# Optimization experiments

Measured on AMD Instinct MI355X. Metric: run time of the kernel, lower is better.

The kernel has to match this reference:

```python
import jax, jax.numpy as jnp
import numpy as np

B, T, C, H = 128, 256, 64, 128  # batch, seq_len, num_channels, hidden_size


def setup_inputs() -> dict:
    key = jax.random.key(0)
    ks = jax.random.split(key, 7)
    s = 1.0 / np.sqrt(H)  # PyTorch LSTM/Linear init bound
    x = jax.random.normal(ks[0], (B, T, C), dtype=jnp.float32)
    # Per-channel LSTM weights (input_size=1). Gate order i,f,g,o like PyTorch.
    w_ih = jax.random.uniform(ks[1], (C, 4 * H), jnp.float32, -s, s)      # [C,4H] (input is scalar)
    w_hh = jax.random.uniform(ks[2], (C, 4 * H, H), jnp.float32, -s, s)   # [C,4H,H]
    b_ih = jax.random.uniform(ks[3], (C, 4 * H), jnp.float32, -s, s)
    b_hh = jax.random.uniform(ks[4], (C, 4 * H), jnp.float32, -s, s)
    # Per-channel Linear(H, 1) head.
    w_fc = jax.random.uniform(ks[5], (C, H), jnp.float32, -s, s)
    b_fc = jax.random.uniform(ks[6], (C,), jnp.float32, -s, s)
    return {"x": x, "w_ih": w_ih, "w_hh": w_hh, "b_ih": b_ih,
            "b_hh": b_hh, "w_fc": w_fc, "b_fc": b_fc}


def reference(x, w_ih, w_hh, b_ih, b_hh, w_fc, b_fc):
    # x: [B,T,C]. All C channel-LSTMs run as one batched recurrence over [B,C].
    b = b_ih + b_hh  # [C,4H]
    xt = jnp.transpose(x, (1, 0, 2))  # [T,B,C] for scan over time
    h0 = jnp.zeros((x.shape[0], x.shape[2], w_hh.shape[-1]), x.dtype)  # [B,C,H]
    c0 = h0

    def step(carry, x_t):
        h, c = carry  # [B,C,H]
        # scalar input times per-channel input weights + recurrent GEMM
        gates = x_t[..., None] * w_ih + jnp.einsum('bch,cgh->bcg', h, w_hh) + b  # [B,C,4H]
        i, f, g, o = jnp.split(gates, 4, axis=-1)
        i = jax.nn.sigmoid(i)
        f = jax.nn.sigmoid(f)
        g = jnp.tanh(g)
        o = jax.nn.sigmoid(o)
        c_new = f * c + i * g
        h_new = o * jnp.tanh(c_new)
        return (h_new, c_new), None

    (hT, _), _ = jax.lax.scan(step, (h0, c0), xt)
    # Per-channel linear head on the last hidden state -> [B,C]
    return jnp.einsum('bch,ch->bc', hT, w_fc) + b_fc
```

## Files before the change

### kernel.cpp

```cpp
#include <hip/hip_runtime.h>
#include <hip/hip_bf16.h>

typedef __bf16 bf16_t;
typedef bf16_t bf16x8 __attribute__((ext_vector_type(8)));
typedef float f32x4 __attribute__((ext_vector_type(4)));

#define B_   128
#define T_   256
#define C_   64
#define H_   128
#define G_   512
#define BT   16
#define XS   20
#define HBUF 2048

#define K1 1.4426950408889634f
#define K2 2.8853900817779268f

__global__ __launch_bounds__(512, 4) void lstm_fused(
    const float* __restrict__ x,
    const float* __restrict__ w_ih,
    const float* __restrict__ w_hh,
    const float* __restrict__ b_ih,
    const float* __restrict__ b_hh,
    const float* __restrict__ w_fc,
    const float* __restrict__ b_fc,
    float* __restrict__ out)
{
    const int c    = blockIdx.x & (C_ - 1);
    const int bt   = blockIdx.x >> 6;
    const int b0   = bt * BT;
    const int tid  = threadIdx.x;
    const int w    = tid >> 6;
    const int lane = tid & 63;
    const int l16  = lane & 15;
    const int lg   = lane >> 4;

    __shared__ __align__(16) bf16_t h_lds[2 * HBUF];
    __shared__ __align__(16) float x_lds[T_ * XS];

    for (int i = tid; i < HBUF; i += 512) ((uint32_t*)h_lds)[i] = 0u;
    for (int i = tid; i < BT * T_; i += 512) {
        const int bl = i >> 8, t = i & 255;
        x_lds[t * XS + bl] = x[(size_t)(b0 + bl) * (T_ * C_) + (size_t)t * C_ + c];
    }

    bf16x8 bw[4][4];
    float  bias[4], wih[4];
    #pragma unroll
    for (int q = 0; q < 4; ++q) {
        const int n = q * 128 + w * 16 + l16;
        bias[q] = b_ih[c * G_ + n] + b_hh[c * G_ + n];
        wih[q]  = w_ih[c * G_ + n];
        #pragma unroll
        for (int kk = 0; kk < 4; ++kk) {
            const int k0 = kk * 32 + lg * 8;
            const float4 wa = *(const float4*)&w_hh[((size_t)(c * G_ + n)) * H_ + k0];
            const float4 wb = *(const float4*)&w_hh[((size_t)(c * G_ + n)) * H_ + k0 + 4];
            bf16x8 g;
            g[0] = (bf16_t)wa.x; g[1] = (bf16_t)wa.y; g[2] = (bf16_t)wa.z; g[3] = (bf16_t)wa.w;
            g[4] = (bf16_t)wb.x; g[5] = (bf16_t)wb.y; g[6] = (bf16_t)wb.z; g[7] = (bf16_t)wb.w;
            bw[q][kk] = g;
        }
    }

    float cst[4] = {0.f, 0.f, 0.f, 0.f};

    __syncthreads();

    const int a_off  = l16 * 8;
    const int wbase  = (w * 2 + (l16 >> 3)) * 128 + lg * 32 + (l16 & 7);

    auto step = [&](const int RD, const int WR, const int t) {
        const f32x4 xv = *(const f32x4*)&x_lds[t * XS + lg * 4];

        bf16x8 a[4];
        #pragma unroll
        for (int kk = 0; kk < 4; ++kk)
            a[kk] = *(const bf16x8*)&h_lds[RD + (kk * 4 + lg) * 128 + a_off];

        f32x4 acc[4];
        #pragma unroll
        for (int q = 0; q < 4; ++q)
            #pragma unroll
            for (int r = 0; r < 4; ++r)
                acc[q][r] = fmaf(xv[r], wih[q], bias[q]);

        #pragma unroll
        for (int q = 0; q < 4; ++q)
            #pragma unroll
            for (int kk = 0; kk < 4; ++kk)
                acc[q] = __builtin_amdgcn_mfma_f32_16x16x32_bf16(a[kk], bw[q][kk], acc[q], 0, 0, 0);

        #pragma unroll
        for (int r = 0; r < 4; ++r) {
            const float ei = __builtin_amdgcn_exp2f(-K1 * acc[0][r]);
            const float ef = __builtin_amdgcn_exp2f(-K1 * acc[1][r]);
            const float eg = __builtin_amdgcn_exp2f( K2 * acc[2][r]);
            const float eo = __builtin_amdgcn_exp2f(-K1 * acc[3][r]);
            const float A  = 1.f + ei, D = 1.f + ef, Bb = 1.f + eg, O = 1.f + eo;
            const float AB = A * Bb;
            const float r1 = __builtin_amdgcn_rcpf(D * AB);
            const float cn = fmaf(D, eg - 1.f, cst[r] * AB) * r1;
            cst[r] = cn;
            float m2 = K2 * cn;
            m2 = fminf(fmaxf(m2, -60.f), 60.f);
            const float ec = __builtin_amdgcn_exp2f(m2);
            const float r2 = __builtin_amdgcn_rcpf(O * (1.f + ec));
            const float hv = (ec - 1.f) * r2;
            h_lds[WR + wbase + r * 8] = (bf16_t)hv;
        }
        __syncthreads();
    };

    for (int t = 0; t < T_; t += 2) {
        step(0, HBUF, t);
        step(HBUF, 0, t + 1);
    }

    #pragma unroll
    for (int rr = 0; rr < 2; ++rr) {
        const int row = w * 2 + rr;
        const int eaddr = (lane >> 2) * 128 + row * 8 + (lane & 3) * 2;
        const float h0 = (float)h_lds[eaddr];
        const float h1 = (float)h_lds[eaddr + 1];
        const float2 wf = *(const float2*)&w_fc[c * H_ + 2 * lane];
        float p = h0 * wf.x + h1 * wf.y;
        #pragma unroll
        for (int off = 32; off; off >>= 1) p += __shfl_xor(p, off);
        if (lane == 0) out[(size_t)(b0 + row) * C_ + c] = p + b_fc[c];
    }
}

extern "C" void kernel_launch(void* const* d_in, const int* in_sizes, int n_in,
                              void* d_out, int out_size, void* d_ws, size_t ws_size,
                              hipStream_t stream) {
    const float* x    = (const float*)d_in[0];
    const float* w_ih = (const float*)d_in[1];
    const float* w_hh = (const float*)d_in[2];
    const float* b_ih = (const float*)d_in[3];
    const float* b_hh = (const float*)d_in[4];
    const float* w_fc = (const float*)d_in[5];
    const float* b_fc = (const float*)d_in[6];
    float* out = (float*)d_out;

    dim3 grid(C_ * (B_ / BT));
    dim3 block(512);
    lstm_fused<<<grid, block, 0, stream>>>(x, w_ih, w_hh, b_ih, b_hh, w_fc, b_fc, out);
}
```

Baseline: 387.6 us.

## Fold input projection and bias into an extra MFMA, prescale gate weights

Moves the scalar input times w_ih plus bias term into an additional bf16 MFMA. A and B operands are built from hi/lo bf16 splits of x, w_ih and bias so precision is kept. The activation scales (-log2e, 2log2e) are folded into the weights so the gate nonlinearities skip a multiply. The elementwise math is also rewritten with packed float2 vectors so the compiler can emit packed FP32 ops. This cuts VALU work per step on the serial recurrence path, at the cost of four extra MFMAs and some operand-packing overhead per step.

Measured after the change: 347.5 us. 10.4% less time.

```diff
diff --git a/kernel.cpp b/kernel.cpp
--- a/kernel.cpp
+++ b/kernel.cpp
@@ -4,6 +4,7 @@
 typedef __bf16 bf16_t;
 typedef bf16_t bf16x8 __attribute__((ext_vector_type(8)));
 typedef float f32x4 __attribute__((ext_vector_type(4)));
+typedef float f32x2 __attribute__((ext_vector_type(2)));
 
 #define B_   128
 #define T_   256
@@ -11,11 +12,22 @@
 #define H_   128
 #define G_   512
 #define BT   16
-#define XS   20
 #define HBUF 2048
 
 #define K1 1.4426950408889634f
 #define K2 2.8853900817779268f
+
+union AF { bf16x8 v; uint32_t w[4]; };
+
+__device__ __forceinline__ uint32_t cvt_pk_bf16(float a, float b) {
+    uint32_t r; asm("v_cvt_pk_bf16_f32 %0, %1, %2" : "=v"(r) : "v"(a), "v"(b)); return r;
+}
+__device__ __forceinline__ f32x2 exp2v(f32x2 z) {
+    f32x2 r; r.x = __builtin_amdgcn_exp2f(z.x); r.y = __builtin_amdgcn_exp2f(z.y); return r;
+}
+__device__ __forceinline__ f32x2 rcpv(f32x2 z) {
+    f32x2 r; r.x = __builtin_amdgcn_rcpf(z.x); r.y = __builtin_amdgcn_rcpf(z.y); return r;
+}
 
 __global__ __launch_bounds__(512, 4) void lstm_fused(
     const float* __restrict__ x,
@@ -35,80 +47,102 @@
     const int lane = tid & 63;
     const int l16  = lane & 15;
     const int lg   = lane >> 4;
+    const bool lg0 = (lg == 0);
 
     __shared__ __align__(16) bf16_t h_lds[2 * HBUF];
-    __shared__ __align__(16) float x_lds[T_ * XS];
+    __shared__ __align__(16) float x_lds[T_ * BT];
 
     for (int i = tid; i < HBUF; i += 512) ((uint32_t*)h_lds)[i] = 0u;
     for (int i = tid; i < BT * T_; i += 512) {
         const int bl = i >> 8, t = i & 255;
-        x_lds[t * XS + bl] = x[(size_t)(b0 + bl) * (T_ * C_) + (size_t)t * C_ + c];
+        x_lds[t * BT + bl] = x[(size_t)(b0 + bl) * (T_ * C_) + (size_t)t * C_ + c];
     }
 
     bf16x8 bw[4][4];
-    float  bias[4], wih[4];
+    AF     augb[4];
     #pragma unroll
     for (int q = 0; q < 4; ++q) {
+        const float s = (q == 2) ? K2 : -K1;
         const int n = q * 128 + w * 16 + l16;
-        bias[q] = b_ih[c * G_ + n] + b_hh[c * G_ + n];
-        wih[q]  = w_ih[c * G_ + n];
         #pragma unroll
         for (int kk = 0; kk < 4; ++kk) {
             const int k0 = kk * 32 + lg * 8;
             const float4 wa = *(const float4*)&w_hh[((size_t)(c * G_ + n)) * H_ + k0];
             const float4 wb = *(const float4*)&w_hh[((size_t)(c * G_ + n)) * H_ + k0 + 4];
             bf16x8 g;
-            g[0] = (bf16_t)wa.x; g[1] = (bf16_t)wa.y; g[2] = (bf16_t)wa.z; g[3] = (bf16_t)wa.w;
-            g[4] = (bf16_t)wb.x; g[5] = (bf16_t)wb.y; g[6] = (bf16_t)wb.z; g[7] = (bf16_t)wb.w;
+            g[0] = (bf16_t)(s * wa.x); g[1] = (bf16_t)(s * wa.y);
+            g[2] = (bf16_t)(s * wa.z); g[3] = (bf16_t)(s * wa.w);
+            g[4] = (bf16_t)(s * wb.x); g[5] = (bf16_t)(s * wb.y);
+            g[6] = (bf16_t)(s * wb.z); g[7] = (bf16_t)(s * wb.w);
             bw[q][kk] = g;
         }
+        const float wv = s * w_ih[c * G_ + n];
+        const bf16_t wh = (bf16_t)wv;
+        const bf16_t wl = (bf16_t)(wv - (float)wh);
+        const float bb = s * (b_ih[c * G_ + n] + b_hh[c * G_ + n]);
+        const bf16_t bh = (bf16_t)bb;
+        const bf16_t bl2 = (bf16_t)(bb - (float)bh);
+        bf16x8 f;
+        #pragma unroll
+        for (int e = 0; e < 8; ++e) f[e] = (bf16_t)0.0f;
+        if (lg0) { f[0] = wh; f[1] = wl; f[2] = wh; f[3] = bh; f[4] = bl2; }
+        augb[q].v = f;
     }
 
     float cst[4] = {0.f, 0.f, 0.f, 0.f};
+    const f32x4 zc = {0.f, 0.f, 0.f, 0.f};
+    const f32x2 one2 = {1.f, 1.f};
 
     __syncthreads();
 
-    const int a_off  = l16 * 8;
-    const int wbase  = (w * 2 + (l16 >> 3)) * 128 + lg * 32 + (l16 & 7);
+    const int a_off = l16 * 8;
+    const int wbase = (w * 2 + (l16 >> 3)) * 128 + lg * 32 + (l16 & 7);
 
     auto step = [&](const int RD, const int WR, const int t) {
-        const f32x4 xv = *(const f32x4*)&x_lds[t * XS + lg * 4];
-
-        bf16x8 a[4];
-        #pragma unroll
-        for (int kk = 0; kk < 4; ++kk)
-            a[kk] = *(const bf16x8*)&h_lds[RD + (kk * 4 + lg) * 128 + a_off];
+        const float xr = x_lds[t * BT + l16];
+        const uint32_t p0 = cvt_pk_bf16(xr, xr);
+        const float xhf = __uint_as_float(p0 << 16);
+        const uint32_t p1 = cvt_pk_bf16(xr - xhf, 1.0f);
+        AF a4;
+        a4.w[0] = lg0 ? p0 : 0u;
+        a4.w[1] = lg0 ? p1 : 0u;
+        a4.w[2] = lg0 ? 0x00003F80u : 0u;
+        a4.w[3] = 0u;
 
         f32x4 acc[4];
+        {
+            #pragma unroll
+            for (int q = 0; q < 4; ++q)
+                acc[q] = __builtin_amdgcn_mfma_f32_16x16x32_bf16(a4.v, augb[q].v, zc, 0, 0, 0);
+        }
         #pragma unroll
-        for (int q = 0; q < 4; ++q)
+        for (int kk = 0; kk < 4; ++kk) {
+            const bf16x8 a = *(const bf16x8*)&h_lds[RD + (kk * 4 + lg) * 128 + a_off];
             #pragma unroll
-            for (int r = 0; r < 4; ++r)
-                acc[q][r] = fmaf(xv[r], wih[q], bias[q]);
+            for (int q = 0; q < 4; ++q)
+                acc[q] = __builtin_amdgcn_mfma_f32_16x16x32_bf16(a, bw[q][kk], acc[q], 0, 0, 0);
+        }
 
         #pragma unroll
-        for (int q = 0; q < 4; ++q)
-            #pragma unroll
-            for (int kk = 0; kk < 4; ++kk)
-                acc[q] = __builtin_amdgcn_mfma_f32_16x16x32_bf16(a[kk], bw[q][kk], acc[q], 0, 0, 0);
-
-        #pragma unroll
-        for (int r = 0; r < 4; ++r) {
-            const float ei = __builtin_amdgcn_exp2f(-K1 * acc[0][r]);
-            const float ef = __builtin_amdgcn_exp2f(-K1 * acc[1][r]);
-            const float eg = __builtin_amdgcn_exp2f( K2 * acc[2][r]);
-            const float eo = __builtin_amdgcn_exp2f(-K1 * acc[3][r]);
-            const float A  = 1.f + ei, D = 1.f + ef, Bb = 1.f + eg, O = 1.f + eo;
-            const float AB = A * Bb;
-            const float r1 = __builtin_amdgcn_rcpf(D * AB);
-            const float cn = fmaf(D, eg - 1.f, cst[r] * AB) * r1;
-            cst[r] = cn;
-            float m2 = K2 * cn;
-            m2 = fminf(fmaxf(m2, -60.f), 60.f);
-            const float ec = __builtin_amdgcn_exp2f(m2);
-            const float r2 = __builtin_amdgcn_rcpf(O * (1.f + ec));
-            const float hv = (ec - 1.f) * r2;
-            h_lds[WR + wbase + r * 8] = (bf16_t)hv;
+        for (int p = 0; p < 2; ++p) {
+            f32x2 zi = {acc[0][2*p], acc[0][2*p+1]};
+            f32x2 zf = {acc[1][2*p], acc[1][2*p+1]};
+            f32x2 zg = {acc[2][2*p], acc[2][2*p+1]};
+            f32x2 zo = {acc[3][2*p], acc[3][2*p+1]};
+            const f32x2 ei = exp2v(zi), ef = exp2v(zf), eg = exp2v(zg), eo = exp2v(zo);
+            const f32x2 A2 = one2 + ei, D2 = one2 + ef, B2 = one2 + eg, O2 = one2 + eo;
+            const f32x2 AB = A2 * B2;
+            const f32x2 r1 = rcpv(D2 * AB);
+            f32x2 cs = {cst[2*p], cst[2*p+1]};
+            const f32x2 cn = (D2 * (eg - one2) + cs * AB) * r1;
+            cst[2*p] = cn.x; cst[2*p+1] = cn.y;
+            f32x2 m2 = K2 * cn;
+            m2 = __builtin_elementwise_min(__builtin_elementwise_max(m2, f32x2{-60.f,-60.f}), f32x2{60.f,60.f});
+            const f32x2 ec = exp2v(m2);
+            const f32x2 r2 = rcpv(O2 * (one2 + ec));
+            const f32x2 hv = (ec - one2) * r2;
+            h_lds[WR + wbase + (2*p)   * 8] = (bf16_t)hv.x;
+            h_lds[WR + wbase + (2*p+1) * 8] = (bf16_t)hv.y;
         }
         __syncthreads();
     };
```
